# Optimization experiments

Measured on AMD Instinct MI355X. Metric: run time of the kernel, lower is better.

Reference implementation:

```python
import jax, jax.numpy as jnp
import numpy as np

N_NODES = 100000
N_EDGES = 625000
D_IN = 128
D_OUT = 128
N_ETYPES = 64


def setup_inputs() -> dict:
    key = jax.random.key(0)
    k1, k2, k3, k4, k5, k6 = jax.random.split(key, 6)
    node_features = jax.random.normal(k1, (N_NODES, D_IN), dtype=jnp.float32)
    edge_index = jax.random.randint(k2, (2, N_EDGES), 0, N_NODES, dtype=jnp.int64)
    edge_type = jax.random.randint(k3, (N_EDGES,), 0, N_ETYPES, dtype=jnp.int64)
    edge_emb = jax.random.normal(k4, (N_ETYPES, D_OUT), dtype=jnp.float32)
    W = jax.random.normal(k5, (D_IN, D_OUT), dtype=jnp.float32) / np.sqrt(D_IN)
    b = jax.random.normal(k6, (D_OUT,), dtype=jnp.float32) * 0.01
    return {"node_features": node_features, "edge_index": edge_index,
            "edge_type": edge_type, "edge_emb": edge_emb, "W": W, "b": b}


def reference(node_features, edge_index, edge_type, edge_emb, W, b):
    # Linear transform of node features: (N, D_out)
    h = node_features @ W + b
    src, tgt = edge_index[0], edge_index[1]
    # Per-edge message: gather src feature + edge-type embedding  (E, D_out)
    messages = h[src] + edge_emb[edge_type]
    # Scatter-add into target nodes
    aggregated = jax.ops.segment_sum(messages, tgt, num_segments=N_NODES)
    # Self contribution + ReLU
    return jax.nn.relu(aggregated + h)
```

## Files before the change

### kernel.cpp

```cpp
#include <hip/hip_runtime.h>
#include <hip/hip_bf16.h>

#define D 128

typedef __attribute__((ext_vector_type(8))) short short8v;
typedef __attribute__((ext_vector_type(4))) float float4v;

__device__ __forceinline__ unsigned short f2bf(float f) {
  union { float f; unsigned int u; } v; v.f = f;
  unsigned int r = v.u + 0x7fffu + ((v.u >> 16) & 1u);
  return (unsigned short)(r >> 16);
}
__device__ __forceinline__ unsigned int pkbf(float lo, float hi) {
  float2 f; f.x = lo; f.y = hi;
  __hip_bfloat162 v = __float22bfloat162_rn(f);
  union { __hip_bfloat162 b; unsigned int u; } c; c.b = v;
  return c.u;
}
__device__ __forceinline__ float bflo(unsigned int u) {
  union { unsigned int v; float f; } c; c.v = u << 16; return c.f;
}
__device__ __forceinline__ float bfhi(unsigned int u) {
  union { unsigned int v; float f; } c; c.v = u & 0xffff0000u; return c.f;
}

__global__ __launch_bounds__(256) void prep_kernel(
    const float* __restrict__ W, const float* __restrict__ eemb,
    unsigned short* __restrict__ Wt, unsigned short* __restrict__ em_bf,
    unsigned short* __restrict__ h_bf, int* __restrict__ counts,
    int n_nodes) {
  int i = blockIdx.x * 256 + threadIdx.x;
  if (i < D * D) Wt[i] = f2bf(W[(i & 127) * D + (i >> 7)]);
  if (i < 64 * D) em_bf[i] = f2bf(eemb[i]);
  if (i < 64) ((unsigned int*)(h_bf + (size_t)n_nodes * D))[i] = 0u;
  if (i >= 64 && i < 128) ((unsigned int*)(em_bf + 64 * D))[i - 64] = 0u;
  if (i < n_nodes) counts[i] = 0;
}

__global__ __launch_bounds__(256) void gemm_h_kernel(
    const float* __restrict__ nf, const unsigned short* __restrict__ Wt,
    const float* __restrict__ b, unsigned short* __restrict__ h_bf,
    const int* __restrict__ eidx_tgt, int* __restrict__ counts,
    int n_nodes, int n_edges, int epb) {
  const int tid = threadIdx.x;
  const int wv = tid >> 6;
  const int ln = tid & 63;
  const int m = ln & 15;
  const int q = ln >> 4;
  const int node = blockIdx.x * 64 + wv * 16 + m;
  const int row = node < n_nodes ? node : n_nodes - 1;
  const float* xrow = nf + (size_t)row * D;

  short8v bfrag[4];
  #pragma unroll
  for (int kc = 0; kc < 4; ++kc) {
    const float4 x0 = *(const float4*)(xrow + kc * 32 + q * 8);
    const float4 x1 = *(const float4*)(xrow + kc * 32 + q * 8 + 4);
    union { unsigned int u[4]; short8v s; } cv;
    cv.u[0] = pkbf(x0.x, x0.y);
    cv.u[1] = pkbf(x0.z, x0.w);
    cv.u[2] = pkbf(x1.x, x1.y);
    cv.u[3] = pkbf(x1.z, x1.w);
    bfrag[kc] = cv.s;
  }

  float4v acc[8] = {};
  #pragma unroll
  for (int nt = 0; nt < 8; ++nt) {
    const unsigned short* wrow = Wt + (nt * 16 + m) * D + q * 8;
    const short8v a0 = *(const short8v*)(wrow);
    const short8v a1 = *(const short8v*)(wrow + 32);
    const short8v a2 = *(const short8v*)(wrow + 64);
    const short8v a3 = *(const short8v*)(wrow + 96);
    acc[nt] = __builtin_amdgcn_mfma_f32_16x16x32_bf16(a0, bfrag[0], acc[nt], 0, 0, 0);
    acc[nt] = __builtin_amdgcn_mfma_f32_16x16x32_bf16(a1, bfrag[1], acc[nt], 0, 0, 0);
    acc[nt] = __builtin_amdgcn_mfma_f32_16x16x32_bf16(a2, bfrag[2], acc[nt], 0, 0, 0);
    acc[nt] = __builtin_amdgcn_mfma_f32_16x16x32_bf16(a3, bfrag[3], acc[nt], 0, 0, 0);
  }

  if (node < n_nodes) {
    unsigned short* orow = h_bf + (size_t)node * D + q * 4;
    #pragma unroll
    for (int nt = 0; nt < 8; ++nt) {
      const float4 bv = *(const float4*)&b[nt * 16 + q * 4];
      uint2 val;
      val.x = pkbf(acc[nt][0] + bv.x, acc[nt][1] + bv.y);
      val.y = pkbf(acc[nt][2] + bv.z, acc[nt][3] + bv.w);
      *(uint2*)(orow + nt * 16) = val;
    }
  }

  const int ebase = blockIdx.x * epb;
  int eend = ebase + epb;
  if (eend > n_edges) eend = n_edges;
  for (int e = ebase + tid; e < eend; e += 256)
    atomicAdd(&counts[eidx_tgt[e]], 1);
}

__global__ __launch_bounds__(256) void scan1_kernel(
    const int* __restrict__ counts, int* __restrict__ offsets,
    int* __restrict__ blockSums, int n) {
  __shared__ int lds[256];
  const int tid = threadIdx.x;
  const int base = blockIdx.x * 1024 + tid * 4;
  int v[4];
  #pragma unroll
  for (int k = 0; k < 4; ++k) v[k] = (base + k < n) ? counts[base + k] : 0;
  int s = v[0] + v[1] + v[2] + v[3];
  lds[tid] = s;
  for (int off = 1; off < 256; off <<= 1) {
    __syncthreads();
    int t = (tid >= off) ? lds[tid - off] : 0;
    __syncthreads();
    lds[tid] += t;
  }
  __syncthreads();
  int run = lds[tid] - s;
  #pragma unroll
  for (int k = 0; k < 4; ++k) {
    if (base + k < n) offsets[base + k] = run;
    run += v[k];
  }
  if (tid == 255) blockSums[blockIdx.x] = lds[255];
}

__global__ __launch_bounds__(256) void scan23_kernel(
    int* __restrict__ offsets, int* __restrict__ cursor,
    const int* __restrict__ blockSums, int nb, int n, int n_edges) {
  __shared__ int lds[256];
  const int tid = threadIdx.x;
  const int bid = blockIdx.x;
  lds[tid] = (tid < bid && tid < nb) ? blockSums[tid] : 0;
  __syncthreads();
  #pragma unroll
  for (int off = 128; off > 0; off >>= 1) {
    if (tid < off) lds[tid] += lds[tid + off];
    __syncthreads();
  }
  const int add = lds[0];
  const int base = bid * 1024 + tid * 4;
  #pragma unroll
  for (int k = 0; k < 4; ++k) {
    int i = base + k;
    if (i < n) {
      int o = offsets[i] + add;
      offsets[i] = o;
      cursor[i] = o;
    }
  }
  if (bid == 0 && tid == 0) offsets[n] = n_edges;
}

__global__ __launch_bounds__(256) void scatter_kernel(
    const int* __restrict__ eidx, const int* __restrict__ etype,
    int* __restrict__ cursor, unsigned int* __restrict__ packed, int n_edges) {
  const int e0 = (blockIdx.x * 256 + threadIdx.x) * 4;
  if (e0 + 3 < n_edges) {
    const int4 s4 = *(const int4*)&eidx[e0];
    const int4 t4 = *(const int4*)&eidx[n_edges + e0];
    const int4 y4 = *(const int4*)&etype[e0];
    int pos;
    pos = atomicAdd(&cursor[t4.x], 1);
    packed[pos] = (unsigned int)s4.x | ((unsigned int)y4.x << 17);
    pos = atomicAdd(&cursor[t4.y], 1);
    packed[pos] = (unsigned int)s4.y | ((unsigned int)y4.y << 17);
    pos = atomicAdd(&cursor[t4.z], 1);
    packed[pos] = (unsigned int)s4.z | ((unsigned int)y4.z << 17);
    pos = atomicAdd(&cursor[t4.w], 1);
    packed[pos] = (unsigned int)s4.w | ((unsigned int)y4.w << 17);
  } else {
    for (int e = e0; e < n_edges; ++e) {
      const int pos = atomicAdd(&cursor[eidx[n_edges + e]], 1);
      packed[pos] = (unsigned int)eidx[e] | ((unsigned int)etype[e] << 17);
    }
  }
}

__global__ __launch_bounds__(256) void aggregate_kernel(
    const int* __restrict__ offsets, const unsigned int* __restrict__ packed,
    const uint2* __restrict__ e4, const uint2* __restrict__ h4,
    float* __restrict__ out, int n_nodes, int n_edges, unsigned int zero_p) {
  const int gid = blockIdx.x * 256 + threadIdx.x;
  const int lane = threadIdx.x & 63;
  const int half = lane >> 5;
  const int sl = lane & 31;
  const int n = (gid >> 6) * 2 + half;
  if (n >= n_nodes) return;

  const uint2 sb = h4[(size_t)n * 32 + sl];
  float a0 = bflo(sb.x), a1 = bfhi(sb.x), a2 = bflo(sb.y), a3 = bfhi(sb.y);
  float c0 = 0.f, c1 = 0.f, c2 = 0.f, c3 = 0.f;

  int j = offsets[n];
  const int end = offsets[n + 1];
  int trips = (end - j + 3) >> 2;
  int to = __shfl_xor(trips, 32);
  const int T = trips > to ? trips : to;
  const int emax = n_edges - 1;

  for (int t = 0; t < T; ++t, j += 4) {
    const int j1 = j + 1, j2 = j + 2, j3 = j + 3;
    unsigned int p0 = packed[j  <= emax ? j  : emax];
    unsigned int p1 = packed[j1 <= emax ? j1 : emax];
    unsigned int p2 = packed[j2 <= emax ? j2 : emax];
    unsigned int p3 = packed[j3 <= emax ? j3 : emax];
    p0 = (j  < end) ? p0 : zero_p;
    p1 = (j1 < end) ? p1 : zero_p;
    p2 = (j2 < end) ? p2 : zero_p;
    p3 = (j3 < end) ? p3 : zero_p;
    const uint2 g0 = h4[(size_t)(p0 & 0x1FFFFu) * 32 + sl];
    const uint2 g1 = h4[(size_t)(p1 & 0x1FFFFu) * 32 + sl];
    const uint2 g2 = h4[(size_t)(p2 & 0x1FFFFu) * 32 + sl];
    const uint2 g3 = h4[(size_t)(p3 & 0x1FFFFu) * 32 + sl];
    const uint2 e0 = e4[(p0 >> 17) * 32 + sl];
    const uint2 e1 = e4[(p1 >> 17) * 32 + sl];
    const uint2 e2 = e4[(p2 >> 17) * 32 + sl];
    const uint2 e3 = e4[(p3 >> 17) * 32 + sl];
    a0 += bflo(g0.x) + bflo(e0.x); a1 += bfhi(g0.x) + bfhi(e0.x);
    a2 += bflo(g0.y) + bflo(e0.y); a3 += bfhi(g0.y) + bfhi(e0.y);
    c0 += bflo(g1.x) + bflo(e1.x); c1 += bfhi(g1.x) + bfhi(e1.x);
    c2 += bflo(g1.y) + bflo(e1.y); c3 += bfhi(g1.y) + bfhi(e1.y);
    a0 += bflo(g2.x) + bflo(e2.x); a1 += bfhi(g2.x) + bfhi(e2.x);
    a2 += bflo(g2.y) + bflo(e2.y); a3 += bfhi(g2.y) + bfhi(e2.y);
    c0 += bflo(g3.x) + bflo(e3.x); c1 += bfhi(g3.x) + bfhi(e3.x);
    c2 += bflo(g3.y) + bflo(e3.y); c3 += bfhi(g3.y) + bfhi(e3.y);
  }

  float4 r;
  r.x = fmaxf(a0 + c0, 0.f);
  r.y = fmaxf(a1 + c1, 0.f);
  r.z = fmaxf(a2 + c2, 0.f);
  r.w = fmaxf(a3 + c3, 0.f);
  ((float4*)out)[(size_t)n * 32 + sl] = r;
}

extern "C" void kernel_launch(void* const* d_in, const int* in_sizes, int n_in,
                              void* d_out, int out_size, void* d_ws,
                              size_t ws_size, hipStream_t stream) {
  const float* nf   = (const float*)d_in[0];
  const int*   eidx = (const int*)d_in[1];
  const int*   etyp = (const int*)d_in[2];
  const float* eemb = (const float*)d_in[3];
  const float* W    = (const float*)d_in[4];
  const float* b    = (const float*)d_in[5];

  const int n_nodes = in_sizes[0] / D;
  const int n_edges = in_sizes[2];

  float* out = (float*)d_out;

  char* base = (char*)d_ws;
  unsigned short* Wt = (unsigned short*)base;
  unsigned short* em_bf = (unsigned short*)(base + 32768);
  unsigned short* h_bf = (unsigned short*)(base + 65536);
  char* tail = base + 65536 + (size_t)(n_nodes + 1) * D * 2;
  int* counts = (int*)tail;
  int* offsets = counts + n_nodes;
  int* cursor = offsets + (n_nodes + 1);
  int* blockSums = cursor + n_nodes;
  unsigned int* packed = (unsigned int*)(blockSums + 1024);

  const int nb = (n_nodes + 1023) / 1024;
  const int gemmBlocks = (n_nodes + 63) / 64;
  const int epb = (n_edges + gemmBlocks - 1) / gemmBlocks;

  prep_kernel<<<(n_nodes + 255) / 256, 256, 0, stream>>>(W, eemb, Wt, em_bf,
                                                         h_bf, counts, n_nodes);

  gemm_h_kernel<<<gemmBlocks, 256, 0, stream>>>(
      nf, Wt, b, h_bf, eidx + n_edges, counts, n_nodes, n_edges, epb);

  scan1_kernel<<<nb, 256, 0, stream>>>(counts, offsets, blockSums, n_nodes);
  scan23_kernel<<<nb, 256, 0, stream>>>(offsets, cursor, blockSums, nb,
                                        n_nodes, n_edges);

  scatter_kernel<<<(n_edges + 1023) / 1024, 256, 0, stream>>>(
      eidx, etyp, cursor, packed, n_edges);

  const unsigned int zero_p = (unsigned int)n_nodes | (64u << 17);
  const int aggBlocks = (n_nodes + 7) / 8;
  aggregate_kernel<<<aggBlocks, 256, 0, stream>>>(
      offsets, packed, (const uint2*)em_bf, (const uint2*)h_bf, out, n_nodes,
      n_edges, zero_p);
}
```

Baseline: 141.6 us.

## Aggregate raw bf16 features first, then apply linear transform fused in aggregation

Uses linearity to reorder the work: gather-sum the bf16 input features of neighbours and the node itself, then run one MFMA GEMM per 16-node tile inside the aggregation kernel. The bias is added scaled by degree+1, and edge embeddings are summed separately and added after the GEMM. This removes the separate GEMM kernel and the h write-and-read, but changes where bf16 rounding happens (sums are rounded to bf16 before the GEMM), which may affect accuracy. The grid assumes n_nodes is divisible by 16, and the count zeroing moves to a memset.

```diff
diff --git a/kernel.cpp b/kernel.cpp
--- a/kernel.cpp
+++ b/kernel.cpp
@@ -25,75 +25,36 @@
 }
 
 __global__ __launch_bounds__(256) void prep_kernel(
-    const float* __restrict__ W, const float* __restrict__ eemb,
+    const float* __restrict__ nf, const float* __restrict__ W,
+    const float* __restrict__ eemb, unsigned short* __restrict__ x_bf,
     unsigned short* __restrict__ Wt, unsigned short* __restrict__ em_bf,
-    unsigned short* __restrict__ h_bf, int* __restrict__ counts,
-    int n_nodes) {
-  int i = blockIdx.x * 256 + threadIdx.x;
-  if (i < D * D) Wt[i] = f2bf(W[(i & 127) * D + (i >> 7)]);
-  if (i < 64 * D) em_bf[i] = f2bf(eemb[i]);
-  if (i < 64) ((unsigned int*)(h_bf + (size_t)n_nodes * D))[i] = 0u;
-  if (i >= 64 && i < 128) ((unsigned int*)(em_bf + 64 * D))[i - 64] = 0u;
-  if (i < n_nodes) counts[i] = 0;
-}
-
-__global__ __launch_bounds__(256) void gemm_h_kernel(
-    const float* __restrict__ nf, const unsigned short* __restrict__ Wt,
-    const float* __restrict__ b, unsigned short* __restrict__ h_bf,
     const int* __restrict__ eidx_tgt, int* __restrict__ counts,
     int n_nodes, int n_edges, int epb) {
-  const int tid = threadIdx.x;
-  const int wv = tid >> 6;
-  const int ln = tid & 63;
-  const int m = ln & 15;
-  const int q = ln >> 4;
-  const int node = blockIdx.x * 64 + wv * 16 + m;
-  const int row = node < n_nodes ? node : n_nodes - 1;
-  const float* xrow = nf + (size_t)row * D;
-
-  short8v bfrag[4];
-  #pragma unroll
-  for (int kc = 0; kc < 4; ++kc) {
-    const float4 x0 = *(const float4*)(xrow + kc * 32 + q * 8);
-    const float4 x1 = *(const float4*)(xrow + kc * 32 + q * 8 + 4);
-    union { unsigned int u[4]; short8v s; } cv;
-    cv.u[0] = pkbf(x0.x, x0.y);
-    cv.u[1] = pkbf(x0.z, x0.w);
-    cv.u[2] = pkbf(x1.x, x1.y);
-    cv.u[3] = pkbf(x1.z, x1.w);
-    bfrag[kc] = cv.s;
-  }
-
-  float4v acc[8] = {};
-  #pragma unroll
-  for (int nt = 0; nt < 8; ++nt) {
-    const unsigned short* wrow = Wt + (nt * 16 + m) * D + q * 8;
-    const short8v a0 = *(const short8v*)(wrow);
-    const short8v a1 = *(const short8v*)(wrow + 32);
-    const short8v a2 = *(const short8v*)(wrow + 64);
-    const short8v a3 = *(const short8v*)(wrow + 96);
-    acc[nt] = __builtin_amdgcn_mfma_f32_16x16x32_bf16(a0, bfrag[0], acc[nt], 0, 0, 0);
-    acc[nt] = __builtin_amdgcn_mfma_f32_16x16x32_bf16(a1, bfrag[1], acc[nt], 0, 0, 0);
-    acc[nt] = __builtin_amdgcn_mfma_f32_16x16x32_bf16(a2, bfrag[2], acc[nt], 0, 0, 0);
-    acc[nt] = __builtin_amdgcn_mfma_f32_16x16x32_bf16(a3, bfrag[3], acc[nt], 0, 0, 0);
-  }
-
-  if (node < n_nodes) {
-    unsigned short* orow = h_bf + (size_t)node * D + q * 4;
-    #pragma unroll
-    for (int nt = 0; nt < 8; ++nt) {
-      const float4 bv = *(const float4*)&b[nt * 16 + q * 4];
-      uint2 val;
-      val.x = pkbf(acc[nt][0] + bv.x, acc[nt][1] + bv.y);
-      val.y = pkbf(acc[nt][2] + bv.z, acc[nt][3] + bv.w);
-      *(uint2*)(orow + nt * 16) = val;
-    }
-  }
+  const int gid = blockIdx.x * 256 + threadIdx.x;
+  const int stride = gridDim.x * 256;
+
+  const int total8 = n_nodes * (D / 8);
+  const float4* nf4 = (const float4*)nf;
+  uint4* xb4 = (uint4*)x_bf;
+  for (int i = gid; i < total8; i += stride) {
+    const float4 a = nf4[i * 2];
+    const float4 c = nf4[i * 2 + 1];
+    uint4 o;
+    o.x = pkbf(a.x, a.y); o.y = pkbf(a.z, a.w);
+    o.z = pkbf(c.x, c.y); o.w = pkbf(c.z, c.w);
+    xb4[i] = o;
+  }
+
+  if (gid < D * D) Wt[gid] = f2bf(W[(gid & 127) * D + (gid >> 7)]);
+  if (gid < 64 * D) em_bf[gid] = f2bf(eemb[gid]);
+  if (gid < 64) ((unsigned int*)(x_bf + (size_t)n_nodes * D))[gid] = 0u;
+  if (gid >= 64 && gid < 128)
+    ((unsigned int*)(em_bf + 64 * D))[gid - 64] = 0u;
 
   const int ebase = blockIdx.x * epb;
   int eend = ebase + epb;
   if (eend > n_edges) eend = n_edges;
-  for (int e = ebase + tid; e < eend; e += 256)
+  for (int e = ebase + threadIdx.x; e < eend; e += 256)
     atomicAdd(&counts[eidx_tgt[e]], 1);
 }
 
@@ -176,23 +137,33 @@
   }
 }
 
-__global__ __launch_bounds__(256) void aggregate_kernel(
+__global__ __launch_bounds__(512) void agg_gemm_kernel(
     const int* __restrict__ offsets, const unsigned int* __restrict__ packed,
-    const uint2* __restrict__ e4, const uint2* __restrict__ h4,
+    const uint2* __restrict__ e4, const uint2* __restrict__ x4,
+    const unsigned short* __restrict__ Wt, const float* __restrict__ b,
     float* __restrict__ out, int n_nodes, int n_edges, unsigned int zero_p) {
-  const int gid = blockIdx.x * 256 + threadIdx.x;
-  const int lane = threadIdx.x & 63;
-  const int half = lane >> 5;
-  const int sl = lane & 31;
-  const int n = (gid >> 6) * 2 + half;
-  if (n >= n_nodes) return;
-
-  const uint2 sb = h4[(size_t)n * 32 + sl];
+  __shared__ uint4 sx_l[16 * 16];
+  __shared__ uint4 se_l[16 * 16];
+  __shared__ float deg_l[16];
+
+  const int tid = threadIdx.x;
+  const int w = tid >> 6;
+  const int ln = tid & 63;
+  const int half = ln >> 5;
+  const int sl = ln & 31;
+  const int node16 = w * 2 + half;
+  const int nodeBase = blockIdx.x * 16;
+  const int n = nodeBase + node16;
+
+  const uint2 sb = x4[(size_t)n * 32 + sl];
   float a0 = bflo(sb.x), a1 = bfhi(sb.x), a2 = bflo(sb.y), a3 = bfhi(sb.y);
   float c0 = 0.f, c1 = 0.f, c2 = 0.f, c3 = 0.f;
+  float s0 = 0.f, s1 = 0.f, s2 = 0.f, s3 = 0.f;
+  float u0 = 0.f, u1 = 0.f, u2 = 0.f, u3 = 0.f;
 
   int j = offsets[n];
   const int end = offsets[n + 1];
+  const float degp1 = (float)(end - j) + 1.0f;
   int trips = (end - j + 3) >> 2;
   int to = __shfl_xor(trips, 32);
   const int T = trips > to ? trips : to;
@@ -208,30 +179,63 @@
     p1 = (j1 < end) ? p1 : zero_p;
     p2 = (j2 < end) ? p2 : zero_p;
     p3 = (j3 < end) ? p3 : zero_p;
-    const uint2 g0 = h4[(size_t)(p0 & 0x1FFFFu) * 32 + sl];
-    const uint2 g1 = h4[(size_t)(p1 & 0x1FFFFu) * 32 + sl];
-    const uint2 g2 = h4[(size_t)(p2 & 0x1FFFFu) * 32 + sl];
-    const uint2 g3 = h4[(size_t)(p3 & 0x1FFFFu) * 32 + sl];
+    const uint2 g0 = x4[(size_t)(p0 & 0x1FFFFu) * 32 + sl];
+    const uint2 g1 = x4[(size_t)(p1 & 0x1FFFFu) * 32 + sl];
+    const uint2 g2 = x4[(size_t)(p2 & 0x1FFFFu) * 32 + sl];
+    const uint2 g3 = x4[(size_t)(p3 & 0x1FFFFu) * 32 + sl];
     const uint2 e0 = e4[(p0 >> 17) * 32 + sl];
     const uint2 e1 = e4[(p1 >> 17) * 32 + sl];
     const uint2 e2 = e4[(p2 >> 17) * 32 + sl];
     const uint2 e3 = e4[(p3 >> 17) * 32 + sl];
-    a0 += bflo(g0.x) + bflo(e0.x); a1 += bfhi(g0.x) + bfhi(e0.x);
-    a2 += bflo(g0.y) + bflo(e0.y); a3 += bfhi(g0.y) + bfhi(e0.y);
-    c0 += bflo(g1.x) + bflo(e1.x); c1 += bfhi(g1.x) + bfhi(e1.x);
-    c2 += bflo(g1.y) + bflo(e1.y); c3 += bfhi(g1.y) + bfhi(e1.y);
-    a0 += bflo(g2.x) + bflo(e2.x); a1 += bfhi(g2.x) + bfhi(e2.x);
-    a2 += bflo(g2.y) + bflo(e2.y); a3 += bfhi(g2.y) + bfhi(e2.y);
-    c0 += bflo(g3.x) + bflo(e3.x); c1 += bfhi(g3.x) + bfhi(e3.x);
-    c2 += bflo(g3.y) + bflo(e3.y); c3 += bfhi(g3.y) + bfhi(e3.y);
-  }
-
-  float4 r;
-  r.x = fmaxf(a0 + c0, 0.f);
-  r.y = fmaxf(a1 + c1, 0.f);
-  r.z = fmaxf(a2 + c2, 0.f);
-  r.w = fmaxf(a3 + c3, 0.f);
-  ((float4*)out)[(size_t)n * 32 + sl] = r;
+    a0 += bflo(g0.x); a1 += bfhi(g0.x); a2 += bflo(g0.y); a3 += bfhi(g0.y);
+    s0 += bflo(e0.x); s1 += bfhi(e0.x); s2 += bflo(e0.y); s3 += bfhi(e0.y);
+    c0 += bflo(g1.x); c1 += bfhi(g1.x); c2 += bflo(g1.y); c3 += bfhi(g1.y);
+    u0 += bflo(e1.x); u1 += bfhi(e1.x); u2 += bflo(e1.y); u3 += bfhi(e1.y);
+    a0 += bflo(g2.x); a1 += bfhi(g2.x); a2 += bflo(g2.y); a3 += bfhi(g2.y);
+    s0 += bflo(e2.x); s1 += bfhi(e2.x); s2 += bflo(e2.y); s3 += bfhi(e2.y);
+    c0 += bflo(g3.x); c1 += bfhi(g3.x); c2 += bflo(g3.y); c3 += bfhi(g3.y);
+    u0 += bflo(e3.x); u1 += bfhi(e3.x); u2 += bflo(e3.y); u3 += bfhi(e3.y);
+  }
+
+  {
+    const int byte = (node16 * 256 + sl * 8) ^ ((node16 & 7) << 4);
+    uint2 vx, ve;
+    vx.x = pkbf(a0 + c0, a1 + c1);
+    vx.y = pkbf(a2 + c2, a3 + c3);
+    ve.x = pkbf(s0 + u0, s1 + u1);
+    ve.y = pkbf(s2 + u2, s3 + u3);
+    *(uint2*)((char*)sx_l + byte) = vx;
+    *(uint2*)((char*)se_l + byte) = ve;
+    if (sl == 0) deg_l[node16] = degp1;
+  }
+  __syncthreads();
+
+  const int m = ln & 15;
+  const int q = ln >> 4;
+
+  float4v acc = {};
+  #pragma unroll
+  for (int kc = 0; kc < 4; ++kc) {
+    const short8v av =
+        *(const short8v*)&Wt[(w * 16 + m) * D + kc * 32 + q * 8];
+    const int bbyte = (m * 256 + kc * 64 + q * 16) ^ ((m & 7) << 4);
+    const short8v bv = *(const short8v*)((const char*)sx_l + bbyte);
+    acc = __builtin_amdgcn_mfma_f32_16x16x32_bf16(av, bv, acc, 0, 0, 0);
+  }
+
+  {
+    const int col0 = w * 16 + q * 4;
+    const float4 bv = *(const float4*)&b[col0];
+    const int sbyte = (m * 256 + col0 * 2) ^ ((m & 7) << 4);
+    const uint2 sev = *(const uint2*)((const char*)se_l + sbyte);
+    const float dp1 = deg_l[m];
+    float4 r;
+    r.x = fmaxf(acc[0] + bv.x * dp1 + bflo(sev.x), 0.f);
+    r.y = fmaxf(acc[1] + bv.y * dp1 + bfhi(sev.x), 0.f);
+    r.z = fmaxf(acc[2] + bv.z * dp1 + bflo(sev.y), 0.f);
+    r.w = fmaxf(acc[3] + bv.w * dp1 + bfhi(sev.y), 0.f);
+    *(float4*)&out[(size_t)(nodeBase + m) * D + col0] = r;
+  }
 }
 
 extern "C" void kernel_launch(void* const* d_in, const int* in_sizes, int n_in,
@@ -252,7 +256,7 @@
   char* base = (char*)d_ws;
   unsigned short* Wt = (unsigned short*)base;
   unsigned short* em_bf = (unsigned short*)(base + 32768);
-  unsigned short* h_bf = (unsigned short*)(base + 65536);
+  unsigned short* x_bf = (unsigned short*)(base + 65536);
   char* tail = base + 65536 + (size_t)(n_nodes + 1) * D * 2;
   int* counts = (int*)tail;
   int* offsets = counts + n_nodes;
@@ -261,14 +265,14 @@
   unsigned int* packed = (unsigned int*)(blockSums + 1024);
 
   const int nb = (n_nodes + 1023) / 1024;
-  const int gemmBlocks = (n_nodes + 63) / 64;
-  const int epb = (n_edges + gemmBlocks - 1) / gemmBlocks;
-
-  prep_kernel<<<(n_nodes + 255) / 256, 256, 0, stream>>>(W, eemb, Wt, em_bf,
-                                                         h_bf, counts, n_nodes);
-
-  gemm_h_kernel<<<gemmBlocks, 256, 0, stream>>>(
-      nf, Wt, b, h_bf, eidx + n_edges, counts, n_nodes, n_edges, epb);
+  const int prepBlocks = 2048;
+  const int epb = (n_edges + prepBlocks - 1) / prepBlocks;
+
+  (void)hipMemsetAsync(counts, 0, (size_t)n_nodes * 4, stream);
+
+  prep_kernel<<<prepBlocks, 256, 0, stream>>>(nf, W, eemb, x_bf, Wt, em_bf,
+                                              eidx + n_edges, counts,
+                                              n_nodes, n_edges, epb);
 
   scan1_kernel<<<nb, 256, 0, stream>>>(counts, offsets, blockSums, n_nodes);
   scan23_kernel<<<nb, 256, 0, stream>>>(offsets, cursor, blockSums, nb,
@@ -278,8 +282,7 @@
       eidx, etyp, cursor, packed, n_edges);
 
   const unsigned int zero_p = (unsigned int)n_nodes | (64u << 17);
-  const int aggBlocks = (n_nodes + 7) / 8;
-  aggregate_kernel<<<aggBlocks, 256, 0, stream>>>(
-      offsets, packed, (const uint2*)em_bf, (const uint2*)h_bf, out, n_nodes,
-      n_edges, zero_p);
-}
+  agg_gemm_kernel<<<n_nodes / 16, 512, 0, stream>>>(
+      offsets, packed, (const uint2*)em_bf, (const uint2*)x_bf, Wt, b, out,
+      n_nodes, n_edges, zero_p);
+}
```

After: 145.6 us. +2.8%, slower.
